# Kernel tuning notes

Measured on AMD Instinct MI355X. Metric: run time of the kernel, lower is better.

## Reference

```python
import jax, jax.numpy as jnp
import numpy as np

E = 192      # embed_dim
DI = 384     # d_inner = 2*E (mamba default expand=2)
S = 16       # d_state
R = 12       # dt_rank = ceil(E/16)
DEPTH = 4
STRIDE = 4
P = 400      # num_patches = 1600/4
NC = 20
BATCH = 32
EPS = 1e-5


def _rmsnorm(x, w):
    x = x.astype(jnp.float32)
    return x * jax.lax.rsqrt(jnp.mean(x * x, axis=-1, keepdims=True) + EPS) * w


def _mamba_mixer(h, in_w, cw, cb, xpw, dtw, dtb, a_log, d_skip, ow):
    # h: [B, L, E]
    Bsz, Ln, _ = h.shape
    xz = jnp.einsum('ble,de->bld', h, in_w)            # [B,L,2*DI]
    xm, z = xz[..., :DI], xz[..., DI:]
    # causal depthwise conv1d, kernel 4 (left pad 3, truncate to L)
    xp = jnp.pad(xm, ((0, 0), (3, 0), (0, 0)))
    xc = sum(xp[:, k:k + Ln, :] * cw[:, k] for k in range(4)) + cb
    xc = jax.nn.silu(xc)
    xdb = jnp.einsum('bld,rd->blr', xc, xpw)           # [B,L,R+2S]
    dt = jax.nn.softplus(jnp.einsum('blr,dr->bld', xdb[..., :R], dtw) + dtb)
    Bm = xdb[..., R:R + S]
    Cm = xdb[..., R + S:]
    A = -jnp.exp(a_log)                                # [DI,S]

    def step(hst, inp):
        dt_t, b_t, c_t, u_t = inp                      # [B,DI],[B,S],[B,S],[B,DI]
        dA = jnp.exp(dt_t[:, :, None] * A)             # [B,DI,S]
        hst = dA * hst + (dt_t * u_t)[:, :, None] * b_t[:, None, :]
        y_t = jnp.einsum('bdn,bn->bd', hst, c_t)
        return hst, y_t

    h0 = jnp.zeros((Bsz, DI, S), xc.dtype)
    xs = (dt.transpose(1, 0, 2), Bm.transpose(1, 0, 2), Cm.transpose(1, 0, 2), xc.transpose(1, 0, 2))
    _, ys = jax.lax.scan(step, h0, xs)
    y = ys.transpose(1, 0, 2) + xc * d_skip
    y = y * jax.nn.silu(z)
    return jnp.einsum('bld,ed->ble', y, ow)


def _forward(imgs, patch_w, patch_b, cls_token, pos_embed, cnn_w, cnn_b, norm_w,
             in_proj_w, conv_w, conv_b, x_proj_w, dt_proj_w, dt_proj_b, A_log, D,
             out_proj_w, norm_f_w, head_w, head_b):
    Bsz = imgs.shape[0]
    # StrideEmbed: conv1d kernel=stride=4 == reshape + matmul
    x = imgs.reshape(Bsz, P, STRIDE)
    x = jnp.einsum('blk,ek->ble', x, patch_w[:, 0, :]) + patch_b   # [B,P,E]
    x = x + pos_embed[:, :-1, :]
    # depthwise conv1d k=3 pad=1 over length
    xp = jnp.pad(x, ((0, 0), (1, 1), (0, 0)))
    x = sum(xp[:, k:k + P, :] * cnn_w[:, 0, k] for k in range(3)) + cnn_b
    cls = cls_token + pos_embed[:, -1, :]                           # [1,1,E]
    x = jnp.concatenate([x, jnp.broadcast_to(cls, (Bsz, 1, E))], axis=1)  # [B,401,E]

    hidden = x
    residual = None
    for i in range(DEPTH):
        residual = hidden if residual is None else residual + hidden
        hn = _rmsnorm(residual, norm_w[i])
        hidden = _mamba_mixer(hn, in_proj_w[i], conv_w[i], conv_b[i], x_proj_w[i],
                              dt_proj_w[i], dt_proj_b[i], A_log[i], D[i], out_proj_w[i])
    out = _rmsnorm(hidden + residual, norm_f_w)
    v_sem = out[:, -1, :]
    return v_sem @ head_w.T + head_b


def setup_inputs() -> dict:
    key = jax.random.key(0)
    ks = jax.random.split(key, 12)
    n = lambda k, shp, s=0.02: jax.random.normal(k, shp, dtype=jnp.float32) * s
    return {
        'imgs': jax.random.normal(ks[0], (BATCH, 1, 40, 40), jnp.float32),
        'patch_w': n(ks[1], (E, 1, STRIDE), 0.3),
        'patch_b': jnp.zeros((E,), jnp.float32),
        'cls_token': n(ks[2], (1, 1, E)),
        'pos_embed': n(ks[3], (1, P + 1, E)),
        'cnn_w': n(ks[4], (E, 1, 3), 0.3),
        'cnn_b': jnp.zeros((E,), jnp.float32),
        'norm_w': jnp.ones((DEPTH, E), jnp.float32),
        'in_proj_w': n(ks[5], (DEPTH, 2 * DI, E), 0.05),
        'conv_w': n(ks[6], (DEPTH, DI, 4), 0.3),
        'conv_b': jnp.zeros((DEPTH, DI), jnp.float32),
        'x_proj_w': n(ks[7], (DEPTH, R + 2 * S, DI), 0.05),
        'dt_proj_w': n(ks[8], (DEPTH, DI, R), 0.3),
        'dt_proj_b': jnp.log(jnp.expm1(jax.random.uniform(ks[9], (DEPTH, DI), minval=0.001, maxval=0.1))),
        'A_log': jnp.log(jnp.broadcast_to(jnp.arange(1, S + 1, dtype=jnp.float32), (DEPTH, DI, S))),
        'D': jnp.ones((DEPTH, DI), jnp.float32),
        'out_proj_w': n(ks[10], (DEPTH, E, DI), 0.05),
        'norm_f_w': jnp.ones((E,), jnp.float32),
        'head_w': n(ks[11], (NC, E)),
        'head_b': jnp.zeros((NC,), jnp.float32),
    }


def reference(imgs, patch_w, patch_b, cls_token, pos_embed, cnn_w, cnn_b, norm_w,
              in_proj_w, conv_w, conv_b, x_proj_w, dt_proj_w, dt_proj_b, A_log, D,
              out_proj_w, norm_f_w, head_w, head_b):
    return _forward(imgs, patch_w, patch_b, cls_token, pos_embed, cnn_w, cnn_b, norm_w,
                    in_proj_w, conv_w, conv_b, x_proj_w, dt_proj_w, dt_proj_b, A_log, D,
                    out_proj_w, norm_f_w, head_w, head_b)
```

## Files before the change

kernel.cpp:

```cpp
#include <hip/hip_runtime.h>
#include <math.h>

#define E 192
#define DI 384
#define S 16
#define R 12
#define DEPTH 4
#define P 400
#define NC 20
#define BATCH 32
#define L 401
#define NTOK (BATCH * L)
#define CH 32
#define NCH 13

using short8 = __attribute__((ext_vector_type(8))) short;
using float4v = __attribute__((ext_vector_type(4))) float;

__device__ __forceinline__ float siluf(float x) {
    return x / (1.f + __expf(-x));
}
__device__ __forceinline__ float softplusf(float x) {
    return (x > 20.f) ? x : log1pf(__expf(x));
}
__device__ __forceinline__ unsigned short f2bf(float x) {
    unsigned int u = __float_as_uint(x);
    unsigned int r = 0x7fffu + ((u >> 16) & 1u);
    return (unsigned short)((u + r) >> 16);
}
__device__ __forceinline__ float bf2f(unsigned short v) {
    return __uint_as_float(((unsigned int)v) << 16);
}

__global__ void k_embed(const float* __restrict__ imgs, const float* __restrict__ patch_w,
                        const float* __restrict__ patch_b, const float* __restrict__ cls_token,
                        const float* __restrict__ pos_embed, const float* __restrict__ cnn_w,
                        const float* __restrict__ cnn_b, float* __restrict__ resid) {
    int idx = blockIdx.x * blockDim.x + threadIdx.x;
    if (idx >= NTOK * E) return;
    int e = idx % E;
    int bl = idx / E;
    int l = bl % L;
    int b = bl / L;
    float out;
    if (l == P) {
        out = cls_token[e] + pos_embed[(size_t)P * E + e];
    } else {
        float w0 = patch_w[e * 4 + 0], w1 = patch_w[e * 4 + 1];
        float w2 = patch_w[e * 4 + 2], w3 = patch_w[e * 4 + 3];
        float pb = patch_b[e];
        const float* ib = imgs + (size_t)b * 1600;
        auto xe = [&](int ll) -> float {
            const float* ip = ib + ll * 4;
            return ip[0] * w0 + ip[1] * w1 + ip[2] * w2 + ip[3] * w3 + pb +
                   pos_embed[(size_t)ll * E + e];
        };
        float c0 = cnn_w[e * 3 + 0], c1 = cnn_w[e * 3 + 1], c2 = cnn_w[e * 3 + 2];
        float acc = cnn_b[e] + xe(l) * c1;
        if (l > 0) acc += xe(l - 1) * c0;
        if (l < P - 1) acc += xe(l + 1) * c2;
        out = acc;
    }
    resid[idx] = out;
}

__global__ void k_rmsnorm(const float* __restrict__ resid, unsigned short* __restrict__ hn,
                          const float* __restrict__ w) {
    int wave = blockIdx.x * (blockDim.x >> 6) + (threadIdx.x >> 6);
    int lane = threadIdx.x & 63;
    if (wave >= NTOK) return;
    size_t base = (size_t)wave * E;
    float v[3];
    float ss = 0.f;
#pragma unroll
    for (int j = 0; j < 3; j++) {
        int e = lane + j * 64;
        float r = resid[base + e];
        v[j] = r;
        ss += r * r;
    }
#pragma unroll
    for (int off = 32; off > 0; off >>= 1) ss += __shfl_xor(ss, off, 64);
    float scale = rsqrtf(ss * (1.f / (float)E) + 1e-5f);
#pragma unroll
    for (int j = 0; j < 3; j++) {
        int e = lane + j * 64;
        hn[base + e] = f2bf(v[j] * scale * w[e]);
    }
}

__global__ void k_prep(const float* __restrict__ in_proj_w, const float* __restrict__ x_proj_w,
                       const float* __restrict__ out_proj_w, const float* __restrict__ A_log,
                       const float* __restrict__ dt_proj_w,
                       unsigned short* __restrict__ w_in, unsigned short* __restrict__ w_x,
                       unsigned short* __restrict__ w_out, float* __restrict__ negA,
                       float* __restrict__ dtw_t) {
    const int n1 = DEPTH * 2 * DI * E;
    const int n2 = DEPTH * 44 * DI;
    const int n3 = DEPTH * E * DI;
    const int n4 = DEPTH * DI * S;
    const int n5 = DEPTH * DI * R;
    int idx = blockIdx.x * blockDim.x + threadIdx.x;
    if (idx < n1) {
        w_in[idx] = f2bf(in_proj_w[idx]);
    } else if (idx < n1 + n2) {
        int i = idx - n1;
        w_x[i] = f2bf(x_proj_w[i]);
    } else if (idx < n1 + n2 + n3) {
        int i = idx - n1 - n2;
        w_out[i] = f2bf(out_proj_w[i]);
    } else if (idx < n1 + n2 + n3 + n4) {
        int i = idx - n1 - n2 - n3;
        int layer = i / (DI * S);
        int rem = i % (DI * S);
        int n = rem / DI;
        int d = rem % DI;
        negA[i] = -__expf(A_log[(size_t)layer * DI * S + d * S + n]);
    } else if (idx < n1 + n2 + n3 + n4 + n5) {
        int i = idx - n1 - n2 - n3 - n4;
        int layer = i / (DI * R);
        int rem = i % (DI * R);
        int r = rem / DI;
        int d = rem % DI;
        dtw_t[i] = dt_proj_w[(size_t)layer * DI * R + d * R + r];
    }
}

__global__ void k_flag(const float* __restrict__ negA, int* __restrict__ flag) {
    int idx = blockIdx.x * blockDim.x + threadIdx.x;
    if (idx >= DEPTH * DI) return;
    int layer = idx / DI;
    int d = idx % DI;
    const float* base = negA + (size_t)layer * DI * S;
    float a0 = base[d];
    bool ok = true;
#pragma unroll
    for (int n = 1; n < S; n++) {
        float an = base[n * DI + d];
        ok = ok && (fabsf(an - (float)(n + 1) * a0) <= 1e-5f * fabsf(an));
    }
    flag[idx] = ok ? 1 : 0;
}

template <int BM, int BN, int BK, int EPI>
__global__ __launch_bounds__(256) void k_gemm_bf16(const unsigned short* __restrict__ A,
                                                   const unsigned short* __restrict__ W,
                                                   float* __restrict__ C,
                                                   unsigned short* __restrict__ XM,
                                                   unsigned short* __restrict__ Z,
                                                   int M, int N, int K) {
    constexpr int PADK = BK + 8;
    constexpr int MT = BM / 32, NT = BN / 32;
    __shared__ unsigned short As[BM][PADK];
    __shared__ unsigned short Bs[BN][PADK];
    int tid = threadIdx.x;
    int m0 = blockIdx.y * BM, n0 = blockIdx.x * BN;
    int wave = tid >> 6, lane = tid & 63;
    int row16 = lane & 15, quad = lane >> 4;
    int wm0 = (wave >> 1) * (BM / 2), wn0 = (wave & 1) * (BN / 2);

    float4v acc[MT][NT];
#pragma unroll
    for (int i = 0; i < MT; i++)
#pragma unroll
        for (int j = 0; j < NT; j++) acc[i][j] = (float4v){0.f, 0.f, 0.f, 0.f};

    for (int k0 = 0; k0 < K; k0 += BK) {
#pragma unroll
        for (int idx = tid * 8; idx < BM * BK; idx += 256 * 8) {
            int row = idx / BK, col = idx % BK;
            int gm = m0 + row;
            short8 v;
            if (gm < M)
                v = *(const short8*)&A[(size_t)gm * K + k0 + col];
            else
                v = (short8)0;
            *(short8*)&As[row][col] = v;
        }
#pragma unroll
        for (int idx = tid * 8; idx < BN * BK; idx += 256 * 8) {
            int row = idx / BK, col = idx % BK;
            int gn = n0 + row;
            short8 v;
            if (gn < N)
                v = *(const short8*)&W[(size_t)gn * K + k0 + col];
            else
                v = (short8)0;
            *(short8*)&Bs[row][col] = v;
        }
        __syncthreads();
#pragma unroll
        for (int kk = 0; kk < BK; kk += 32) {
            int koff = kk + quad * 8;
            short8 af[MT], bfr[NT];
#pragma unroll
            for (int i = 0; i < MT; i++)
                af[i] = *(const short8*)&As[wm0 + i * 16 + row16][koff];
#pragma unroll
            for (int j = 0; j < NT; j++)
                bfr[j] = *(const short8*)&Bs[wn0 + j * 16 + row16][koff];
#pragma unroll
            for (int i = 0; i < MT; i++)
#pragma unroll
                for (int j = 0; j < NT; j++)
                    acc[i][j] = __builtin_amdgcn_mfma_f32_16x16x32_bf16(af[i], bfr[j],
                                                                        acc[i][j], 0, 0, 0);
        }
        __syncthreads();
    }
#pragma unroll
    for (int i = 0; i < MT; i++) {
#pragma unroll
        for (int j = 0; j < NT; j++) {
#pragma unroll
            for (int r = 0; r < 4; r++) {
                int m = m0 + wm0 + i * 16 + quad * 4 + r;
                int n = n0 + wn0 + j * 16 + row16;
                if (m >= M || n >= N) continue;
                float v = acc[i][j][r];
                if (EPI == 0) {
                    C[(size_t)m * N + n] = v;
                } else if (EPI == 1) {
                    if (n < DI)
                        XM[(size_t)m * DI + n] = f2bf(v);
                    else
                        Z[(size_t)m * DI + (n - DI)] = f2bf(v);
                } else {
                    C[(size_t)m * N + n] += v;
                }
            }
        }
    }
}

__global__ void k_conv(const unsigned short* __restrict__ xm_bf, const float* __restrict__ cw,
                       const float* __restrict__ cb, unsigned short* __restrict__ xc_bf) {
    int idx = blockIdx.x * blockDim.x + threadIdx.x;
    if (idx >= NTOK * DI) return;
    int d = idx % DI;
    int bl = idx / DI;
    int l = bl % L;
    int b = bl / L;
    const unsigned short* base = xm_bf + (size_t)b * L * DI + d;
    float acc = cb[d];
#pragma unroll
    for (int k = 0; k < 4; k++) {
        int ll = l - 3 + k;
        if (ll >= 0) acc += bf2f(base[(size_t)ll * DI]) * cw[d * 4 + k];
    }
    xc_bf[idx] = f2bf(siluf(acc));
}

__global__ __launch_bounds__(384) void k_dtpre(
        const float* __restrict__ xdb, const float* __restrict__ dtw_t,
        const float* __restrict__ dtb, float* __restrict__ dtbuf) {
    int tok = blockIdx.x;
    int d = threadIdx.x;
    const float* xr = xdb + (size_t)tok * 44;
    float acc = dtb[d];
#pragma unroll
    for (int r = 0; r < R; r++) acc += xr[r] * dtw_t[r * DI + d];
    dtbuf[(size_t)tok * DI + d] = softplusf(acc);
}

template <bool LAST>
__global__ __launch_bounds__(384) void k_scanA(
        const unsigned short* __restrict__ xc_bf, const float* __restrict__ xdb,
        const float* __restrict__ dtbuf, const float* __restrict__ negA_l,
        const int* __restrict__ flag_l, const float* __restrict__ Dskip,
        float2* __restrict__ ydt, float* __restrict__ hend) {
    int d = threadIdx.x;
    int ch = blockIdx.x;
    int b = blockIdx.y;
    int t0 = ch * CH;
    int t1 = min(t0 + CH, L);
    bool fast = __all(flag_l[d] != 0);
    float a0 = negA_l[d];
    float a[S];
    if (!fast) {
#pragma unroll
        for (int n = 0; n < S; n++) a[n] = negA_l[n * DI + d];
    }
    float dsk = Dskip[d];
    float h[S] = {};
    float dts = 0.f;
    size_t tok0 = (size_t)b * L + t0;
    float dt_nx = dtbuf[tok0 * DI + d];
    float u_nx = bf2f(xc_bf[tok0 * DI + d]);
    float e1_nx = __expf(a0 * dt_nx);
    for (int t = t0; t < t1; t++) {
        size_t tok = (size_t)b * L + t;
        float dtv = dt_nx, e1v = e1_nx, uu = u_nx;
        if (t + 1 < t1) {
            dt_nx = dtbuf[(tok + 1) * DI + d];
            u_nx = bf2f(xc_bf[(tok + 1) * DI + d]);
            e1_nx = __expf(a0 * dt_nx);
        }
        const float* row = xdb + tok * 44;
        dts += dtv;
        float dtu = dtv * uu;
        float y = uu * dsk;
        if (fast) {
            float p = e1v;
#pragma unroll
            for (int n = 0; n < S; n++) {
                h[n] = p * h[n] + dtu * row[R + n];
                y += h[n] * row[R + S + n];
                p *= e1v;
            }
        } else {
#pragma unroll
            for (int n = 0; n < S; n++) {
                float dA = __expf(dtv * a[n]);
                h[n] = dA * h[n] + dtu * row[R + n];
                y += h[n] * row[R + S + n];
            }
        }
        if (!LAST || t == P || t == t1 - 1) ydt[tok * DI + d] = make_float2(y, dts);
    }
    float* he = hend + ((size_t)(b * NCH + ch) * S) * DI + d;
#pragma unroll
    for (int n = 0; n < S; n++) he[n * DI] = h[n];
}

__global__ void k_scanB(const float* __restrict__ hend, const float2* __restrict__ ydt,
                        const float* __restrict__ negA_l, const int* __restrict__ flag_l,
                        float* __restrict__ hinit) {
    int idx = blockIdx.x * blockDim.x + threadIdx.x;
    if (idx >= BATCH * DI) return;
    int d = idx % DI;
    int b = idx / DI;
    bool fast = __all(flag_l[d] != 0);
    float a[S];
#pragma unroll
    for (int n = 0; n < S; n++) a[n] = negA_l[n * DI + d];
    float h[S] = {};
    for (int ch = 0; ch < NCH; ch++) {
        size_t o = ((size_t)(b * NCH + ch) * S) * DI + d;
#pragma unroll
        for (int n = 0; n < S; n++) hinit[o + n * DI] = h[n];
        int tlast = min(ch * CH + CH, L) - 1;
        float dts = ydt[((size_t)b * L + tlast) * DI + d].y;
        if (fast) {
            float e1c = __expf(a[0] * dts);
            float p = e1c;
#pragma unroll
            for (int n = 0; n < S; n++) {
                h[n] = p * h[n] + hend[o + n * DI];
                p *= e1c;
            }
        } else {
#pragma unroll
            for (int n = 0; n < S; n++) h[n] = __expf(dts * a[n]) * h[n] + hend[o + n * DI];
        }
    }
}

__global__ __launch_bounds__(384) void k_fixup(
        const unsigned short* __restrict__ z_bf, const float* __restrict__ xdb,
        const float* __restrict__ negA_l, const int* __restrict__ flag_l,
        const float* __restrict__ hinit, const float2* __restrict__ ydt,
        unsigned short* __restrict__ y_bf) {
    int tok = blockIdx.x;
    int d = threadIdx.x;
    int l = tok % L;
    int b = tok / L;
    int ch = l / CH;
    size_t idx = (size_t)tok * DI + d;
    float2 yd = ydt[idx];
    float y = yd.x;
    if (ch != 0) {
        bool fast = __all(flag_l[d] != 0);
        const float* h0 = hinit + ((size_t)(b * NCH + ch) * S) * DI + d;
        const float* cv = xdb + (size_t)tok * 44 + R + S;
        float dts = yd.y;
        float corr = 0.f;
        if (fast) {
            float e1c = __expf(negA_l[d] * dts);
            float p = e1c;
#pragma unroll
            for (int n = 0; n < S; n++) {
                corr += cv[n] * p * h0[n * DI];
                p *= e1c;
            }
        } else {
#pragma unroll
            for (int n = 0; n < S; n++)
                corr += cv[n] * __expf(negA_l[n * DI + d] * dts) * h0[n * DI];
        }
        y += corr;
    }
    float z = bf2f(z_bf[idx]);
    y_bf[idx] = f2bf(y * siluf(z));
}

__global__ __launch_bounds__(384) void k_fixup_last(
        const unsigned short* __restrict__ z_bf, const float* __restrict__ xdb,
        const float* __restrict__ negA_l, const int* __restrict__ flag_l,
        const float* __restrict__ hinit, const float2* __restrict__ ydt,
        unsigned short* __restrict__ y32) {
    int b = blockIdx.x;
    int d = threadIdx.x;
    int tok = b * L + P;
    int ch = P / CH;
    size_t idx = (size_t)tok * DI + d;
    float2 yd = ydt[idx];
    float y = yd.x;
    {
        bool fast = __all(flag_l[d] != 0);
        const float* h0 = hinit + ((size_t)(b * NCH + ch) * S) * DI + d;
        const float* cv = xdb + (size_t)tok * 44 + R + S;
        float dts = yd.y;
        float corr = 0.f;
        if (fast) {
            float e1c = __expf(negA_l[d] * dts);
            float p = e1c;
#pragma unroll
            for (int n = 0; n < S; n++) {
                corr += cv[n] * p * h0[n * DI];
                p *= e1c;
            }
        } else {
#pragma unroll
            for (int n = 0; n < S; n++)
                corr += cv[n] * __expf(negA_l[n * DI + d] * dts) * h0[n * DI];
        }
        y += corr;
    }
    float z = bf2f(z_bf[idx]);
    y32[(size_t)b * DI + d] = f2bf(y * siluf(z));
}

__global__ void k_head(const float* __restrict__ resid, const float* __restrict__ hidden32,
                       const float* __restrict__ norm_f_w, const float* __restrict__ head_w,
                       const float* __restrict__ head_b, float* __restrict__ out) {
    __shared__ float v[E];
    int b = blockIdx.x;
    int lane = threadIdx.x;
    size_t base = ((size_t)b * L + P) * E;
    float loc[3];
    float ss = 0.f;
#pragma unroll
    for (int j = 0; j < 3; j++) {
        int e = lane + j * 64;
        float x = resid[base + e] + hidden32[(size_t)b * E + e];
        loc[j] = x;
        ss += x * x;
    }
#pragma unroll
    for (int off = 32; off > 0; off >>= 1) ss += __shfl_xor(ss, off, 64);
    float scale = rsqrtf(ss * (1.f / (float)E) + 1e-5f);
#pragma unroll
    for (int j = 0; j < 3; j++) {
        int e = lane + j * 64;
        v[e] = loc[j] * scale * norm_f_w[e];
    }
    __syncthreads();
    if (lane < NC) {
        float acc = head_b[lane];
        for (int e = 0; e < E; e++) acc += v[e] * head_w[lane * E + e];
        out[b * NC + lane] = acc;
    }
}

extern "C" void kernel_launch(void* const* d_in, const int* in_sizes, int n_in,
                              void* d_out, int out_size, void* d_ws, size_t ws_size,
                              hipStream_t stream) {
    const float* imgs      = (const float*)d_in[0];
    const float* patch_w   = (const float*)d_in[1];
    const float* patch_b   = (const float*)d_in[2];
    const float* cls_token = (const float*)d_in[3];
    const float* pos_embed = (const float*)d_in[4];
    const float* cnn_w     = (const float*)d_in[5];
    const float* cnn_b     = (const float*)d_in[6];
    const float* norm_w    = (const float*)d_in[7];
    const float* in_proj_w = (const float*)d_in[8];
    const float* conv_w    = (const float*)d_in[9];
    const float* conv_b    = (const float*)d_in[10];
    const float* x_proj_w  = (const float*)d_in[11];
    const float* dt_proj_w = (const float*)d_in[12];
    const float* dt_proj_b = (const float*)d_in[13];
    const float* A_log     = (const float*)d_in[14];
    const float* Dskip     = (const float*)d_in[15];
    const float* out_proj_w= (const float*)d_in[16];
    const float* norm_f_w  = (const float*)d_in[17];
    const float* head_w    = (const float*)d_in[18];
    const float* head_b    = (const float*)d_in[19];

    float* ws = (float*)d_ws;
    size_t off = 0;
    float* resid  = ws + off; off += (size_t)NTOK * E;
    float* xdb    = ws + off; off += (size_t)NTOK * 44;
    float* dtbuf  = ws + off; off += (size_t)NTOK * DI;
    float* ydt    = ws + off; off += (size_t)NTOK * DI * 2;
    float* hend   = ws + off; off += (size_t)BATCH * NCH * DI * S;
    float* hinit  = ws + off; off += (size_t)BATCH * NCH * DI * S;
    float* negA   = ws + off; off += (size_t)DEPTH * DI * S;
    float* dtw_t  = ws + off; off += (size_t)DEPTH * DI * R;
    float* hid32  = ws + off; off += (size_t)BATCH * E;
    int*   gflag  = (int*)(ws + off); off += (size_t)DEPTH * DI;
    unsigned short* xm_bf  = (unsigned short*)(ws + off); off += (size_t)NTOK * DI / 2;
    unsigned short* z_bf   = (unsigned short*)(ws + off); off += (size_t)NTOK * DI / 2;
    unsigned short* bf_buf = (unsigned short*)(ws + off); off += (size_t)NTOK * DI / 2;
    unsigned short* y32_bf = (unsigned short*)(ws + off); off += (size_t)BATCH * DI / 2 + 16;
    unsigned short* w_in  = (unsigned short*)(ws + off); off += (size_t)DEPTH * 2 * DI * E / 2;
    unsigned short* w_x   = (unsigned short*)(ws + off); off += (size_t)DEPTH * 44 * DI / 2 + 16;
    unsigned short* w_out = (unsigned short*)(ws + off); off += (size_t)DEPTH * E * DI / 2;

    unsigned short* hn_bf = bf_buf;
    unsigned short* xc_bf = bf_buf;
    unsigned short* y_bf  = bf_buf;

    {
        int ntot = DEPTH * (2 * DI * E + 44 * DI + E * DI + DI * S + DI * R);
        k_prep<<<(ntot + 255) / 256, 256, 0, stream>>>(in_proj_w, x_proj_w, out_proj_w, A_log,
                                                       dt_proj_w, w_in, w_x, w_out, negA,
                                                       dtw_t);
        k_flag<<<(DEPTH * DI + 255) / 256, 256, 0, stream>>>(negA, gflag);
    }

    k_embed<<<(NTOK * E) / 256, 256, 0, stream>>>(imgs, patch_w, patch_b, cls_token,
                                                  pos_embed, cnn_w, cnn_b, resid);

    for (int i = 0; i < DEPTH; i++) {
        k_rmsnorm<<<NTOK / 4, 256, 0, stream>>>(resid, hn_bf, norm_w + i * E);

        {
            dim3 g((2 * DI) / 64, (NTOK + 127) / 128);
            k_gemm_bf16<128, 64, 64, 1><<<g, 256, 0, stream>>>(
                hn_bf, w_in + (size_t)i * 2 * DI * E, nullptr, xm_bf, z_bf, NTOK, 2 * DI, E);
        }
        k_conv<<<(NTOK * DI) / 256, 256, 0, stream>>>(xm_bf, conv_w + (size_t)i * DI * 4,
                                                      conv_b + (size_t)i * DI, xc_bf);
        {
            dim3 g(1, NTOK / 32);
            k_gemm_bf16<32, 64, 128, 0><<<g, 256, 0, stream>>>(
                xc_bf, w_x + (size_t)i * 44 * DI, xdb, nullptr, nullptr, NTOK, 44, DI);
        }
        const float* nA = negA + (size_t)i * DI * S;
        const int* fl = gflag + (size_t)i * DI;
        k_dtpre<<<NTOK, 384, 0, stream>>>(xdb, dtw_t + (size_t)i * DI * R,
                                          dt_proj_b + (size_t)i * DI, dtbuf);
        dim3 g(NCH, BATCH);
        if (i < DEPTH - 1) {
            k_scanA<false><<<g, DI, 0, stream>>>(xc_bf, xdb, dtbuf, nA, fl,
                                                 Dskip + (size_t)i * DI, (float2*)ydt, hend);
            k_scanB<<<(BATCH * DI + 255) / 256, 256, 0, stream>>>(hend, (const float2*)ydt,
                                                                  nA, fl, hinit);
            k_fixup<<<NTOK, 384, 0, stream>>>(z_bf, xdb, nA, fl, hinit,
                                              (const float2*)ydt, y_bf);
            dim3 go(E / 64, (NTOK + 63) / 64);
            k_gemm_bf16<64, 64, 128, 2><<<go, 256, 0, stream>>>(
                y_bf, w_out + (size_t)i * E * DI, resid, nullptr, nullptr, NTOK, E, DI);
        } else {
            k_scanA<true><<<g, DI, 0, stream>>>(xc_bf, xdb, dtbuf, nA, fl,
                                                Dskip + (size_t)i * DI, (float2*)ydt, hend);
            k_scanB<<<(BATCH * DI + 255) / 256, 256, 0, stream>>>(hend, (const float2*)ydt,
                                                                  nA, fl, hinit);
            k_fixup_last<<<BATCH, 384, 0, stream>>>(z_bf, xdb, nA, fl, hinit,
                                                    (const float2*)ydt, y32_bf);
            dim3 go(E / 64, 1);
            k_gemm_bf16<32, 64, 128, 0><<<go, 256, 0, stream>>>(
                y32_bf, w_out + (size_t)i * E * DI, hid32, nullptr, nullptr, BATCH, E, DI);
        }
    }

    k_head<<<BATCH, 64, 0, stream>>>(resid, hid32, norm_f_w, head_w, head_b, (float*)d_out);
}
```

Baseline: 729.7 us.

## Fuse chunk-state carry scan into fixup kernel, dropping scanB and hinit buffer

```diff
diff --git a/kernel.cpp b/kernel.cpp
--- a/kernel.cpp
+++ b/kernel.cpp
@@ -323,55 +323,106 @@
     for (int n = 0; n < S; n++) he[n * DI] = h[n];
 }
 
-__global__ void k_scanB(const float* __restrict__ hend, const float2* __restrict__ ydt,
-                        const float* __restrict__ negA_l, const int* __restrict__ flag_l,
-                        float* __restrict__ hinit) {
-    int idx = blockIdx.x * blockDim.x + threadIdx.x;
-    if (idx >= BATCH * DI) return;
-    int d = idx % DI;
-    int b = idx / DI;
-    bool fast = __all(flag_l[d] != 0);
-    float a[S];
-#pragma unroll
-    for (int n = 0; n < S; n++) a[n] = negA_l[n * DI + d];
-    float h[S] = {};
-    for (int ch = 0; ch < NCH; ch++) {
-        size_t o = ((size_t)(b * NCH + ch) * S) * DI + d;
-#pragma unroll
-        for (int n = 0; n < S; n++) hinit[o + n * DI] = h[n];
-        int tlast = min(ch * CH + CH, L) - 1;
-        float dts = ydt[((size_t)b * L + tlast) * DI + d].y;
-        if (fast) {
-            float e1c = __expf(a[0] * dts);
-            float p = e1c;
-#pragma unroll
-            for (int n = 0; n < S; n++) {
-                h[n] = p * h[n] + hend[o + n * DI];
-                p *= e1c;
-            }
-        } else {
-#pragma unroll
-            for (int n = 0; n < S; n++) h[n] = __expf(dts * a[n]) * h[n] + hend[o + n * DI];
-        }
-    }
-}
-
 __global__ __launch_bounds__(384) void k_fixup(
         const unsigned short* __restrict__ z_bf, const float* __restrict__ xdb,
         const float* __restrict__ negA_l, const int* __restrict__ flag_l,
-        const float* __restrict__ hinit, const float2* __restrict__ ydt,
+        const float* __restrict__ hend, const float2* __restrict__ ydt,
         unsigned short* __restrict__ y_bf) {
-    int tok = blockIdx.x;
     int d = threadIdx.x;
-    int l = tok % L;
-    int b = tok / L;
-    int ch = l / CH;
+    int ch = blockIdx.x;
+    int b = blockIdx.y;
+    bool fast = __all(flag_l[d] != 0);
+    float a0 = negA_l[d];
+    float a[S];
+    if (!fast) {
+#pragma unroll
+        for (int n = 0; n < S; n++) a[n] = negA_l[n * DI + d];
+    }
+    float h0[S] = {};
+    for (int c = 0; c < ch; c++) {
+        size_t o = ((size_t)(b * NCH + c) * S) * DI + d;
+        int tlast = min(c * CH + CH, L) - 1;
+        float dts = ydt[((size_t)b * L + tlast) * DI + d].y;
+        if (fast) {
+            float e1c = __expf(a0 * dts);
+            float p = e1c;
+#pragma unroll
+            for (int n = 0; n < S; n++) {
+                h0[n] = p * h0[n] + hend[o + n * DI];
+                p *= e1c;
+            }
+        } else {
+#pragma unroll
+            for (int n = 0; n < S; n++) h0[n] = __expf(dts * a[n]) * h0[n] + hend[o + n * DI];
+        }
+    }
+    int t0 = ch * CH, t1 = min(t0 + CH, L);
+    for (int t = t0; t < t1; t++) {
+        size_t idx = ((size_t)b * L + t) * DI + d;
+        float2 yd = ydt[idx];
+        float y = yd.x;
+        if (ch != 0) {
+            const float* cv = xdb + ((size_t)b * L + t) * 44 + R + S;
+            float dts = yd.y;
+            float corr = 0.f;
+            if (fast) {
+                float e1c = __expf(negA_l[d] * dts);
+                float p = e1c;
+#pragma unroll
+                for (int n = 0; n < S; n++) {
+                    corr += cv[n] * p * h0[n];
+                    p *= e1c;
+                }
+            } else {
+#pragma unroll
+                for (int n = 0; n < S; n++)
+                    corr += cv[n] * __expf(negA_l[n * DI + d] * dts) * h0[n];
+            }
+            y += corr;
+        }
+        float z = bf2f(z_bf[idx]);
+        y_bf[idx] = f2bf(y * siluf(z));
+    }
+}
+
+__global__ __launch_bounds__(384) void k_fixup_last(
+        const unsigned short* __restrict__ z_bf, const float* __restrict__ xdb,
+        const float* __restrict__ negA_l, const int* __restrict__ flag_l,
+        const float* __restrict__ hend, const float2* __restrict__ ydt,
+        unsigned short* __restrict__ y32) {
+    int b = blockIdx.x;
+    int d = threadIdx.x;
+    int tok = b * L + P;
+    const int ch = P / CH;
+    bool fast = __all(flag_l[d] != 0);
+    float a0 = negA_l[d];
+    float a[S];
+    if (!fast) {
+#pragma unroll
+        for (int n = 0; n < S; n++) a[n] = negA_l[n * DI + d];
+    }
+    float h0[S] = {};
+    for (int c = 0; c < ch; c++) {
+        size_t o = ((size_t)(b * NCH + c) * S) * DI + d;
+        int tlast = min(c * CH + CH, L) - 1;
+        float dts = ydt[((size_t)b * L + tlast) * DI + d].y;
+        if (fast) {
+            float e1c = __expf(a0 * dts);
+            float p = e1c;
+#pragma unroll
+            for (int n = 0; n < S; n++) {
+                h0[n] = p * h0[n] + hend[o + n * DI];
+                p *= e1c;
+            }
+        } else {
+#pragma unroll
+            for (int n = 0; n < S; n++) h0[n] = __expf(dts * a[n]) * h0[n] + hend[o + n * DI];
+        }
+    }
     size_t idx = (size_t)tok * DI + d;
     float2 yd = ydt[idx];
     float y = yd.x;
-    if (ch != 0) {
-        bool fast = __all(flag_l[d] != 0);
-        const float* h0 = hinit + ((size_t)(b * NCH + ch) * S) * DI + d;
+    {
         const float* cv = xdb + (size_t)tok * 44 + R + S;
         float dts = yd.y;
         float corr = 0.f;
@@ -380,50 +431,13 @@
             float p = e1c;
 #pragma unroll
             for (int n = 0; n < S; n++) {
-                corr += cv[n] * p * h0[n * DI];
+                corr += cv[n] * p * h0[n];
                 p *= e1c;
             }
         } else {
 #pragma unroll
             for (int n = 0; n < S; n++)
-                corr += cv[n] * __expf(negA_l[n * DI + d] * dts) * h0[n * DI];
-        }
-        y += corr;
-    }
-    float z = bf2f(z_bf[idx]);
-    y_bf[idx] = f2bf(y * siluf(z));
-}
-
-__global__ __launch_bounds__(384) void k_fixup_last(
-        const unsigned short* __restrict__ z_bf, const float* __restrict__ xdb,
-        const float* __restrict__ negA_l, const int* __restrict__ flag_l,
-        const float* __restrict__ hinit, const float2* __restrict__ ydt,
-        unsigned short* __restrict__ y32) {
-    int b = blockIdx.x;
-    int d = threadIdx.x;
-    int tok = b * L + P;
-    int ch = P / CH;
-    size_t idx = (size_t)tok * DI + d;
-    float2 yd = ydt[idx];
-    float y = yd.x;
-    {
-        bool fast = __all(flag_l[d] != 0);
-        const float* h0 = hinit + ((size_t)(b * NCH + ch) * S) * DI + d;
-        const float* cv = xdb + (size_t)tok * 44 + R + S;
-        float dts = yd.y;
-        float corr = 0.f;
-        if (fast) {
-            float e1c = __expf(negA_l[d] * dts);
-            float p = e1c;
-#pragma unroll
-            for (int n = 0; n < S; n++) {
-                corr += cv[n] * p * h0[n * DI];
-                p *= e1c;
-            }
-        } else {
-#pragma unroll
-            for (int n = 0; n < S; n++)
-                corr += cv[n] * __expf(negA_l[n * DI + d] * dts) * h0[n * DI];
+                corr += cv[n] * __expf(negA_l[n * DI + d] * dts) * h0[n];
         }
         y += corr;
     }
@@ -494,7 +508,6 @@
     float* dtbuf  = ws + off; off += (size_t)NTOK * DI;
     float* ydt    = ws + off; off += (size_t)NTOK * DI * 2;
     float* hend   = ws + off; off += (size_t)BATCH * NCH * DI * S;
-    float* hinit  = ws + off; off += (size_t)BATCH * NCH * DI * S;
     float* negA   = ws + off; off += (size_t)DEPTH * DI * S;
     float* dtw_t  = ws + off; off += (size_t)DEPTH * DI * R;
     float* hid32  = ws + off; off += (size_t)BATCH * E;
@@ -545,20 +558,16 @@
         if (i < DEPTH - 1) {
             k_scanA<false><<<g, DI, 0, stream>>>(xc_bf, xdb, dtbuf, nA, fl,
                                                  Dskip + (size_t)i * DI, (float2*)ydt, hend);
-            k_scanB<<<(BATCH * DI + 255) / 256, 256, 0, stream>>>(hend, (const float2*)ydt,
-                                                                  nA, fl, hinit);
-            k_fixup<<<NTOK, 384, 0, stream>>>(z_bf, xdb, nA, fl, hinit,
-                                              (const float2*)ydt, y_bf);
+            k_fixup<<<g, DI, 0, stream>>>(z_bf, xdb, nA, fl, hend,
+                                          (const float2*)ydt, y_bf);
             dim3 go(E / 64, (NTOK + 63) / 64);
             k_gemm_bf16<64, 64, 128, 2><<<go, 256, 0, stream>>>(
                 y_bf, w_out + (size_t)i * E * DI, resid, nullptr, nullptr, NTOK, E, DI);
         } else {
             k_scanA<true><<<g, DI, 0, stream>>>(xc_bf, xdb, dtbuf, nA, fl,
                                                 Dskip + (size_t)i * DI, (float2*)ydt, hend);
-            k_scanB<<<(BATCH * DI + 255) / 256, 256, 0, stream>>>(hend, (const float2*)ydt,
-                                                                  nA, fl, hinit);
-            k_fixup_last<<<BATCH, 384, 0, stream>>>(z_bf, xdb, nA, fl, hinit,
-                                                    (const float2*)ydt, y32_bf);
+            k_fixup_last<<<BATCH, DI, 0, stream>>>(z_bf, xdb, nA, fl, hend,
+                                                   (const float2*)ydt, y32_bf);
             dim3 go(E / 64, 1);
             k_gemm_bf16<32, 64, 128, 0><<<go, 256, 0, stream>>>(
                 y32_bf, w_out + (size_t)i * E * DI, hid32, nullptr, nullptr, BATCH, E, DI);
```

After: 746.8 us. 2.3% more time.
